# Optimization experiments

Measured on AMD Instinct MI355X. Metric: run time of the kernel, lower is better.

The kernel has to match this reference:

```python
import jax, jax.numpy as jnp
import numpy as np
import math

HIDDEN = 2048
N_HEADS = 16
N_KV_HEADS = 4
HEAD_DIM = HIDDEN // N_HEADS  # 128
MAX_POS = 4096
ROPE_THETA = 10000.0
B, S = 2, 2048


def _rope_tables():
    freqs = 1.0 / (ROPE_THETA ** (np.arange(0, HEAD_DIM, 2, dtype=np.float32) / HEAD_DIM))
    t = np.arange(MAX_POS, dtype=np.float32)
    f = np.outer(t, freqs)                      # [MAX_POS, HEAD_DIM/2]
    emb = np.concatenate([f, f], axis=-1)       # [MAX_POS, HEAD_DIM]
    return jnp.asarray(np.cos(emb)), jnp.asarray(np.sin(emb))


def setup_inputs() -> dict:
    key = jax.random.key(0)
    ks = jax.random.split(key, 8)
    kv_dim = N_KV_HEADS * HEAD_DIM
    cos, sin = _rope_tables()
    return {
        "hidden_states": jax.random.normal(ks[0], (B, S, HIDDEN), jnp.float32),
        "attention_mask": jnp.zeros((B, S), jnp.float32),
        "position_ids": jnp.arange(S, dtype=jnp.int64 if jax.config.read('jax_enable_x64') else jnp.int32)[None, :],
        "q_w": jax.random.normal(ks[1], (HIDDEN, HIDDEN), jnp.float32) * 0.02,
        "q_b": jnp.zeros((HIDDEN,), jnp.float32),
        "k_w": jax.random.normal(ks[2], (kv_dim, HIDDEN), jnp.float32) * 0.02,
        "k_b": jnp.zeros((kv_dim,), jnp.float32),
        "v_w": jax.random.normal(ks[3], (kv_dim, HIDDEN), jnp.float32) * 0.02,
        "v_b": jnp.zeros((kv_dim,), jnp.float32),
        "o_w": jax.random.normal(ks[4], (HIDDEN, HIDDEN), jnp.float32) * 0.02,
        "cos": cos,
        "sin": sin,
    }


def _rotate_half(x):
    x1, x2 = jnp.split(x, 2, axis=-1)
    return jnp.concatenate([-x2, x1], axis=-1)


def reference(hidden_states, attention_mask, position_ids, q_w, q_b, k_w, k_b,
              v_w, v_b, o_w, cos, sin):
    b, s, _ = hidden_states.shape
    # projections (torch Linear: y = x @ W.T + b)
    q = jnp.einsum('bsi,oi->bso', hidden_states, q_w) + q_b
    k = jnp.einsum('bsi,oi->bso', hidden_states, k_w) + k_b
    v = jnp.einsum('bsi,oi->bso', hidden_states, v_w) + v_b
    q = q.reshape(b, s, N_HEADS, HEAD_DIM).transpose(0, 2, 1, 3)      # [b,h,s,d]
    k = k.reshape(b, s, N_KV_HEADS, HEAD_DIM).transpose(0, 2, 1, 3)   # [b,kv,s,d]
    v = v.reshape(b, s, N_KV_HEADS, HEAD_DIM).transpose(0, 2, 1, 3)
    # RoPE: gather per-position cos/sin, broadcast over heads
    c = cos[position_ids][:, None, :, :]   # [1,1,s,d]
    sn = sin[position_ids][:, None, :, :]
    q = q * c + _rotate_half(q) * sn
    k = k * c + _rotate_half(k) * sn
    # GQA: repeat-interleave kv heads to match query heads
    g = N_HEADS // N_KV_HEADS
    k = jnp.repeat(k, g, axis=1)
    v = jnp.repeat(v, g, axis=1)
    scores = jnp.einsum('bhqd,bhkd->bhqk', q, k) / math.sqrt(HEAD_DIM)
    scores = scores + attention_mask[:, None, None, :]
    attn = jax.nn.softmax(scores.astype(jnp.float32), axis=-1).astype(q.dtype)
    out = jnp.einsum('bhqk,bhkd->bhqd', attn, v)
    out = out.transpose(0, 2, 1, 3).reshape(b, s, HIDDEN)
    return jnp.einsum('bsi,oi->bso', out, o_w)
```

## Files before the change

kernel.cpp:

```cpp
#include <hip/hip_runtime.h>

#define HIDDEN 2048
#define NH 16
#define NKV 4
#define HD 128
#define Bb 2
#define Ss 2048
#define TOK 4096
#define KVD 512
#define LOG2E 1.4426950408889634f
#define QSCALE (0.08838834764831845f * 1.4426950408889634f)
#define DEFER 11.54f

typedef short short8 __attribute__((ext_vector_type(8)));
typedef float f32x4 __attribute__((ext_vector_type(4)));
typedef float f32x16 __attribute__((ext_vector_type(16)));
typedef unsigned int uint4v __attribute__((ext_vector_type(4)));

#define AS1 __attribute__((address_space(1)))
#define AS3 __attribute__((address_space(3)))

#define BARRIER() asm volatile("s_barrier" ::: "memory")
#define WAITV8()  asm volatile("s_waitcnt vmcnt(8)" ::: "memory")
#define WAITV0()  asm volatile("s_waitcnt vmcnt(0)" ::: "memory")

__device__ __forceinline__ float exp2fast(float x){ return __builtin_amdgcn_exp2f(x); }

__device__ __forceinline__ float bf2f(unsigned short u){
  union { unsigned int i; float f; } x; x.i = ((unsigned int)u) << 16; return x.f;
}
__device__ __forceinline__ unsigned short f2bf(float f){
  union { float f; unsigned int i; } x; x.f = f;
  unsigned int r = x.i + 0x7FFFu + ((x.i >> 16) & 1u);
  return (unsigned short)(r >> 16);
}
__device__ __forceinline__ unsigned int cvtpk(float a, float b){
  unsigned int r;
  asm("v_cvt_pk_bf16_f32 %0, %1, %2" : "=v"(r) : "v"(a), "v"(b));
  return r;
}
__device__ __forceinline__ void gld_lds16(const void* g, void* l){
  __builtin_amdgcn_global_load_lds((const AS1 void*)g, (AS3 void*)l, 16, 0, 0);
}

#define R0 2097152
#define R1 3145728
#define R2 3407872
#define R3 3670016
#define R4 4718592
__global__ void cvt_all(const float* __restrict__ s0, const float* __restrict__ s1,
                        const float* __restrict__ s2, const float* __restrict__ s3,
                        const float* __restrict__ s4, unsigned short* __restrict__ dst){
  int i = blockIdx.x * 256 + threadIdx.x;
  const float* src; int off;
  if      (i < R0){ src = s0; off = 0;  }
  else if (i < R1){ src = s1; off = R0; }
  else if (i < R2){ src = s2; off = R1; }
  else if (i < R3){ src = s3; off = R2; }
  else            { src = s4; off = R3; }
  float4 v = reinterpret_cast<const float4*>(src)[i - off];
  ushort4 o;
  o.x = f2bf(v.x); o.y = f2bf(v.y); o.z = f2bf(v.z); o.w = f2bf(v.w);
  reinterpret_cast<ushort4*>(dst)[i] = o;
}

__global__ __launch_bounds__(256, 2) void gemm_nt(
    const unsigned short* __restrict__ A,
    const unsigned short* __restrict__ Bw,
    const float* __restrict__ bias,
    const float* __restrict__ bias2,
    unsigned short* __restrict__ Cb,
    float* __restrict__ Cf,
    unsigned short* __restrict__ vT,
    int M, int N, int K, int ldc)
{
  __shared__ unsigned short lds[2][2][128*64];
  const int tid  = threadIdx.x;
  const int lane = tid & 63;
  const int w  = tid >> 6;
  const int wr = w >> 1, wc = w & 1;
  const int row0 = blockIdx.x * 128;
  const int col0 = blockIdx.y * 128;
  const int fr  = lane & 15;
  const int g16 = lane >> 4;
  const int l8  = lane >> 3;
  const int slot = lane & 7;

  const f32x4 vzero = {0.f, 0.f, 0.f, 0.f};
  f32x4 acc[4][4];
#pragma unroll
  for (int m = 0; m < 4; m++)
#pragma unroll
    for (int n = 0; n < 4; n++) acc[m][n] = vzero;

  auto STAGE = [&](int buf, int kt){
#pragma unroll
    for (int i = 0; i < 4; i++){
      int r = w*32 + i*8 + l8;
      gld_lds16(A  + (size_t)(row0 + r)*K + kt*64 + ((slot ^ (r & 7)) << 3),
                &lds[buf][0][w*2048 + i*512 + lane*8]);
    }
#pragma unroll
    for (int i = 0; i < 4; i++){
      int r = w*32 + i*8 + l8;
      gld_lds16(Bw + (size_t)(col0 + r)*K + kt*64 + ((slot ^ (r & 7)) << 3),
                &lds[buf][1][w*2048 + i*512 + lane*8]);
    }
  };

  const int NT = K >> 6;
  STAGE(0, 0);
  STAGE(1, 1);
  WAITV8();
  BARRIER();

  for (int kt = 0; kt < NT; kt++){
    const int cur = kt & 1;
    const unsigned short* Al = &lds[cur][0][0];
    const unsigned short* Bl = &lds[cur][1][0];
#pragma unroll
    for (int ks = 0; ks < 2; ks++){
      short8 af[4], bf[4];
#pragma unroll
      for (int m = 0; m < 4; m++){
        int r = wr*64 + m*16 + fr;
        af[m] = *(const short8*)&Al[r*64 + (((ks*4 + g16) ^ (r & 7)) << 3)];
      }
#pragma unroll
      for (int n = 0; n < 4; n++){
        int r = wc*64 + n*16 + fr;
        bf[n] = *(const short8*)&Bl[r*64 + (((ks*4 + g16) ^ (r & 7)) << 3)];
      }
      __builtin_amdgcn_s_setprio(1);
#pragma unroll
      for (int m = 0; m < 4; m++)
#pragma unroll
        for (int n = 0; n < 4; n++)
          acc[m][n] = __builtin_amdgcn_mfma_f32_16x16x32_bf16(af[m], bf[n], acc[m][n], 0, 0, 0);
      __builtin_amdgcn_s_setprio(0);
    }
    if (kt == NT - 1) break;
    BARRIER();
    if (kt + 2 < NT){
      STAGE(cur, kt + 2);
      WAITV8();
    } else {
      WAITV0();
    }
    BARRIER();
  }

  const int rr = g16 * 4;
#pragma unroll
  for (int n = 0; n < 4; n++){
    int col = col0 + wc*64 + n*16 + fr;
    float bv = 0.f;
    if (bias) bv = (bias2 && col >= 512) ? bias2[col - 512] : bias[col];
    if (vT && col >= 512){
#pragma unroll
      for (int m = 0; m < 4; m++){
        int row = row0 + wr*64 + m*16 + rr;
        ushort4 pk;
        pk.x = f2bf(acc[m][n][0] + bv); pk.y = f2bf(acc[m][n][1] + bv);
        pk.z = f2bf(acc[m][n][2] + bv); pk.w = f2bf(acc[m][n][3] + bv);
        *reinterpret_cast<ushort4*>(&vT[(size_t)(col - 512) * TOK + row]) = pk;
      }
    } else {
#pragma unroll
      for (int m = 0; m < 4; m++){
        int row = row0 + wr*64 + m*16 + rr;
#pragma unroll
        for (int r = 0; r < 4; r++){
          float v = acc[m][n][r] + bv;
          if (Cf) Cf[(size_t)(row + r) * ldc + col] = v;
          else    Cb[(size_t)(row + r) * ldc + col] = f2bf(v);
        }
      }
    }
  }
}

__global__ void rope_kernel(unsigned short* __restrict__ q, unsigned short* __restrict__ k,
                            const int* __restrict__ pos,
                            const float* __restrict__ cosT, const float* __restrict__ sinT)
{
  int idx = blockIdx.x * blockDim.x + threadIdx.x;
  const int qN = TOK * NH * 64;
  if (idx < qN){
    int d  = idx & 63;
    int hh = (idx >> 6) & (NH - 1);
    int t  = idx >> 10;
    int p  = pos[t & (Ss - 1)];
    float c = cosT[p * HD + d], s = sinT[p * HD + d];
    unsigned short* base = q + (size_t)t * HIDDEN + hh * HD;
    float lo = bf2f(base[d]), hi = bf2f(base[d + 64]);
    base[d]      = f2bf((lo * c - hi * s) * QSCALE);
    base[d + 64] = f2bf((hi * c + lo * s) * QSCALE);
  } else {
    int j  = idx - qN;
    int d  = j & 63;
    int hh = (j >> 6) & (NKV - 1);
    int t  = j >> 8;
    int p  = pos[t & (Ss - 1)];
    float c = cosT[p * HD + d], s = sinT[p * HD + d];
    unsigned short* base = k + (size_t)t * KVD + hh * HD;
    float lo = bf2f(base[d]), hi = bf2f(base[d + 64]);
    base[d]      = f2bf(lo * c - hi * s);
    base[d + 64] = f2bf(hi * c + lo * s);
  }
}

__global__ __launch_bounds__(512, 2) void attn_kernel(
    const unsigned short* __restrict__ Q,
    const unsigned short* __restrict__ Kb,
    const unsigned short* __restrict__ Vt,
    const float* __restrict__ mask,
    unsigned short* __restrict__ O)
{
  __shared__ unsigned short Klds[64*128];
  __shared__ unsigned short Vlds[128*64];

  const int tid = threadIdx.x, lane = tid & 63, wid = tid >> 6;
  const int qt = blockIdx.x, kvh = blockIdx.y, b = blockIdx.z;
  const int head = kvh*4 + (wid >> 1);
  const int q0 = lane & 31;
  const int h  = lane >> 5;
  const int tokQ = b*Ss + qt*64 + (wid & 1)*32;

  short8 qf[8];
#pragma unroll
  for (int ds = 0; ds < 8; ds++)
    qf[ds] = *(const short8*)(Q + (size_t)(tokQ + q0)*HIDDEN + head*HD + ds*16 + h*8);

  f32x16 oacc[4];
#pragma unroll
  for (int dblk = 0; dblk < 4; dblk++)
#pragma unroll
    for (int r = 0; r < 16; r++) oacc[dblk][r] = 0.f;
  float mrow = -1e30f, lrow = 0.f;

  const float* maskrow = mask + b*Ss;

  const int kk0 = tid >> 4;
  const int kd  = tid & 15;
  const int dv0 = tid >> 3;
  const int vk  = tid & 7;

  const size_t kgbase = (size_t)(b*Ss)*KVD + (size_t)kvh*HD;
  const size_t vgbase = (size_t)(kvh*HD)*TOK + (size_t)(b*Ss);

  short8 kpre[2], vpre[2];
#pragma unroll
  for (int i = 0; i < 2; i++){
    kpre[i] = *(const short8*)(Kb + kgbase + (size_t)(kk0 + i*32)*KVD + kd*8);
    vpre[i] = *(const short8*)(Vt + vgbase + (size_t)(dv0 + i*64)*TOK + vk*8);
  }

  for (int kt = 0; kt < Ss/64; kt++){
    if (kt) __syncthreads();
#pragma unroll
    for (int i = 0; i < 2; i++){
      int kk = kk0 + i*32;
      *(short8*)&Klds[kk*128 + ((kd*8) ^ ((kk & 7) << 3))] = kpre[i];
      int dv = dv0 + i*64;
      *(short8*)&Vlds[dv*64 + ((vk*8) ^ ((dv & 7) << 3))] = vpre[i];
    }
    __syncthreads();
    if (kt + 1 < Ss/64){
      const int tok = (kt + 1)*64;
#pragma unroll
      for (int i = 0; i < 2; i++){
        kpre[i] = *(const short8*)(Kb + kgbase + (size_t)(tok + kk0 + i*32)*KVD + kd*8);
        vpre[i] = *(const short8*)(Vt + vgbase + (size_t)(dv0 + i*64)*TOK + tok + vk*8);
      }
    }

    f32x16 st0, st1;
#pragma unroll
    for (int r = 0; r < 16; r++){ st0[r] = 0.f; st1[r] = 0.f; }
    __builtin_amdgcn_s_setprio(1);
#pragma unroll
    for (int ds = 0; ds < 8; ds++){
      short8 kf0 = *(const short8*)&Klds[(q0     )*128 + ((ds*16 + h*8) ^ ((q0 & 7) << 3))];
      short8 kf1 = *(const short8*)&Klds[(32 + q0)*128 + ((ds*16 + h*8) ^ ((q0 & 7) << 3))];
      st0 = __builtin_amdgcn_mfma_f32_32x32x16_bf16(kf0, qf[ds], st0, 0, 0, 0);
      st1 = __builtin_amdgcn_mfma_f32_32x32x16_bf16(kf1, qf[ds], st1, 0, 0, 0);
    }
    __builtin_amdgcn_s_setprio(0);

    float p[32];
#pragma unroll
    for (int g2 = 0; g2 < 4; g2++){
      f32x4 m0 = *(const f32x4*)(maskrow + kt*64      + g2*8 + h*4);
      f32x4 m1 = *(const f32x4*)(maskrow + kt*64 + 32 + g2*8 + h*4);
#pragma unroll
      for (int r = 0; r < 4; r++){
        p[g2*4 + r]      = st0[g2*4 + r] + m0[r] * LOG2E;
        p[16 + g2*4 + r] = st1[g2*4 + r] + m1[r] * LOG2E;
      }
    }

    float vmax = p[0];
#pragma unroll
    for (int i = 1; i < 32; i++) vmax = fmaxf(vmax, p[i]);
    vmax = fmaxf(vmax, __shfl_xor(vmax, 32));
    if (__any(vmax > mrow + DEFER)){
      float mnew = fmaxf(mrow, vmax);
      float sc = exp2fast(mrow - mnew);
      mrow = mnew; lrow *= sc;
#pragma unroll
      for (int reg = 0; reg < 16; reg++){
        float scr = __shfl(sc, (reg & 3) + 8*(reg >> 2) + 4*h);
#pragma unroll
        for (int dblk = 0; dblk < 4; dblk++) oacc[dblk][reg] *= scr;
      }
    }
    float rs = 0.f;
#pragma unroll
    for (int i = 0; i < 32; i++){ p[i] = exp2fast(p[i] - mrow); rs += p[i]; }
    rs += __shfl_xor(rs, 32);
    lrow += rs;

    unsigned int pk[8][2];
#pragma unroll
    for (int G = 0; G < 8; G++){
      pk[G][0] = cvtpk(p[G*4 + 0], p[G*4 + 1]);
      pk[G][1] = cvtpk(p[G*4 + 2], p[G*4 + 3]);
    }
    short8 pa[4];
#pragma unroll
    for (int ks = 0; ks < 4; ks++){
      const int ia = 4*(ks >> 1) + 2*(ks & 1);
      unsigned int A0 = pk[ia][0],   A1 = pk[ia][1];
      unsigned int B0 = pk[ia+1][0], B1 = pk[ia+1][1];
      unsigned int s0 = h ? A0 : B0, s1 = h ? A1 : B1;
      unsigned int r0 = (unsigned int)__shfl_xor((int)s0, 32);
      unsigned int r1 = (unsigned int)__shfl_xor((int)s1, 32);
      uint4v w = { h ? r0 : A0, h ? r1 : A1, h ? B0 : r0, h ? B1 : r1 };
      pa[ks] = __builtin_bit_cast(short8, w);
    }

    __builtin_amdgcn_s_setprio(1);
#pragma unroll
    for (int dblk = 0; dblk < 4; dblk++){
#pragma unroll
      for (int ks = 0; ks < 4; ks++){
        short8 vb = *(const short8*)&Vlds[(dblk*32 + q0)*64 + ((ks*16 + h*8) ^ ((q0 & 7) << 3))];
        oacc[dblk] = __builtin_amdgcn_mfma_f32_32x32x16_bf16(pa[ks], vb, oacc[dblk], 0, 0, 0);
      }
    }
    __builtin_amdgcn_s_setprio(0);
  }

  float inv = 1.0f / lrow;
#pragma unroll
  for (int reg = 0; reg < 16; reg++){
    const int crow = (reg & 3) + 8*(reg >> 2) + 4*h;
    float invr = __shfl(inv, crow);
    int row = tokQ + crow;
#pragma unroll
    for (int dblk = 0; dblk < 4; dblk++)
      O[(size_t)row*HIDDEN + head*HD + dblk*32 + q0] = f2bf(oacc[dblk][reg] * invr);
  }
}

extern "C" void kernel_launch(void* const* d_in, const int* in_sizes, int n_in,
                              void* d_out, int out_size, void* d_ws, size_t ws_size,
                              hipStream_t stream)
{
  (void)in_sizes; (void)n_in; (void)out_size; (void)ws_size;
  const float* hs   = (const float*)d_in[0];
  const float* mask = (const float*)d_in[1];
  const int*   pos  = (const int*)d_in[2];
  const float* qw   = (const float*)d_in[3];
  const float* qb   = (const float*)d_in[4];
  const float* kw   = (const float*)d_in[5];
  const float* kb   = (const float*)d_in[6];
  const float* vw   = (const float*)d_in[7];
  const float* vb   = (const float*)d_in[8];
  const float* ow   = (const float*)d_in[9];
  const float* cosT = (const float*)d_in[10];
  const float* sinT = (const float*)d_in[11];
  float* out = (float*)d_out;

  unsigned short* ws  = (unsigned short*)d_ws;
  unsigned short* hsB = ws;
  unsigned short* qwB = hsB + (size_t)TOK * HIDDEN;
  unsigned short* kwB = qwB + (size_t)HIDDEN * HIDDEN;
  unsigned short* vwB = kwB + (size_t)KVD * HIDDEN;
  unsigned short* owB = vwB + (size_t)KVD * HIDDEN;
  unsigned short* qB  = owB + (size_t)HIDDEN * HIDDEN;
  unsigned short* kB  = qB  + (size_t)TOK * HIDDEN;
  unsigned short* vTB = kB  + (size_t)TOK * KVD;
  unsigned short* aoB = vTB + (size_t)KVD * TOK;
  (void)vwB;

  cvt_all<<<R4 / 256, 256, 0, stream>>>(hs, qw, kw, vw, ow, ws);

  gemm_nt<<<dim3(TOK/128, HIDDEN/128), 256, 0, stream>>>(hsB, qwB, qb, nullptr, qB, nullptr, nullptr, TOK, HIDDEN, HIDDEN, HIDDEN);
  gemm_nt<<<dim3(TOK/128, 1024/128),   256, 0, stream>>>(hsB, kwB, kb, vb, kB, nullptr, vTB, TOK, 1024, HIDDEN, KVD);

  {
    int total = TOK * NH * 64 + TOK * NKV * 64;
    rope_kernel<<<total / 256, 256, 0, stream>>>(qB, kB, pos, cosT, sinT);
  }

  attn_kernel<<<dim3(Ss/64, NKV, Bb), 512, 0, stream>>>(qB, kB, vTB, mask, aoB);

  gemm_nt<<<dim3(TOK/128, HIDDEN/128), 256, 0, stream>>>(aoB, owB, nullptr, nullptr, nullptr, out, nullptr, TOK, HIDDEN, HIDDEN, HIDDEN);
}
```

Baseline: 223.8 us.

## Double-buffer K/V tiles in LDS and shrink attention blocks to 32 queries

The attention kernel now uses two LDS buffers for K and V tiles, writing the next tile while computing on the current one. This cuts the per-tile barriers from two to one. Blocks shrink to 4 waves covering 32 query rows across the 4 heads of a KV group, and the grid doubles. This aims to overlap loads with MFMA work, at the cost of twice the LDS per block and twice the K/V global reads per query.

```diff
diff --git a/kernel.cpp b/kernel.cpp
--- a/kernel.cpp
+++ b/kernel.cpp
@@ -210,22 +210,22 @@
   }
 }
 
-__global__ __launch_bounds__(512, 2) void attn_kernel(
+__global__ __launch_bounds__(256, 2) void attn_kernel(
     const unsigned short* __restrict__ Q,
     const unsigned short* __restrict__ Kb,
     const unsigned short* __restrict__ Vt,
     const float* __restrict__ mask,
     unsigned short* __restrict__ O)
 {
-  __shared__ unsigned short Klds[64*128];
-  __shared__ unsigned short Vlds[128*64];
+  __shared__ unsigned short Klds[2][64*128];
+  __shared__ unsigned short Vlds[2][128*64];
 
   const int tid = threadIdx.x, lane = tid & 63, wid = tid >> 6;
   const int qt = blockIdx.x, kvh = blockIdx.y, b = blockIdx.z;
-  const int head = kvh*4 + (wid >> 1);
+  const int head = kvh*4 + wid;
   const int q0 = lane & 31;
   const int h  = lane >> 5;
-  const int tokQ = b*Ss + qt*64 + (wid & 1)*32;
+  const int tokQ = b*Ss + qt*32;
 
   short8 qf[8];
 #pragma unroll
@@ -249,31 +249,34 @@
   const size_t kgbase = (size_t)(b*Ss)*KVD + (size_t)kvh*HD;
   const size_t vgbase = (size_t)(kvh*HD)*TOK + (size_t)(b*Ss);
 
-  short8 kpre[2], vpre[2];
-#pragma unroll
-  for (int i = 0; i < 2; i++){
-    kpre[i] = *(const short8*)(Kb + kgbase + (size_t)(kk0 + i*32)*KVD + kd*8);
-    vpre[i] = *(const short8*)(Vt + vgbase + (size_t)(dv0 + i*64)*TOK + vk*8);
-  }
-
-  for (int kt = 0; kt < Ss/64; kt++){
-    if (kt) __syncthreads();
-#pragma unroll
-    for (int i = 0; i < 2; i++){
-      int kk = kk0 + i*32;
-      *(short8*)&Klds[kk*128 + ((kd*8) ^ ((kk & 7) << 3))] = kpre[i];
-      int dv = dv0 + i*64;
-      *(short8*)&Vlds[dv*64 + ((vk*8) ^ ((dv & 7) << 3))] = vpre[i];
-    }
-    __syncthreads();
-    if (kt + 1 < Ss/64){
-      const int tok = (kt + 1)*64;
-#pragma unroll
-      for (int i = 0; i < 2; i++){
-        kpre[i] = *(const short8*)(Kb + kgbase + (size_t)(tok + kk0 + i*32)*KVD + kd*8);
-        vpre[i] = *(const short8*)(Vt + vgbase + (size_t)(dv0 + i*64)*TOK + tok + vk*8);
-      }
-    }
+  short8 kpre[4], vpre[4];
+  auto LOADREG = [&](int tok){
+#pragma unroll
+    for (int i = 0; i < 4; i++){
+      kpre[i] = *(const short8*)(Kb + kgbase + (size_t)(tok + kk0 + i*16)*KVD + kd*8);
+      vpre[i] = *(const short8*)(Vt + vgbase + (size_t)(dv0 + i*32)*TOK + tok + vk*8);
+    }
+  };
+  auto WRITELDS = [&](int buf){
+#pragma unroll
+    for (int i = 0; i < 4; i++){
+      int kk = kk0 + i*16;
+      *(short8*)&Klds[buf][kk*128 + ((kd*8) ^ ((kk & 7) << 3))] = kpre[i];
+      int dv = dv0 + i*32;
+      *(short8*)&Vlds[buf][dv*64 + ((vk*8) ^ ((dv & 7) << 3))] = vpre[i];
+    }
+  };
+
+  const int NT = Ss/64;
+  LOADREG(0);
+  WRITELDS(0);
+  LOADREG(64);
+  __syncthreads();
+
+  for (int kt = 0; kt < NT; kt++){
+    const int buf = kt & 1;
+    if (kt + 1 < NT) WRITELDS(buf ^ 1);
+    if (kt + 2 < NT) LOADREG((kt + 2)*64);
 
     f32x16 st0, st1;
 #pragma unroll
@@ -281,8 +284,8 @@
     __builtin_amdgcn_s_setprio(1);
 #pragma unroll
     for (int ds = 0; ds < 8; ds++){
-      short8 kf0 = *(const short8*)&Klds[(q0     )*128 + ((ds*16 + h*8) ^ ((q0 & 7) << 3))];
-      short8 kf1 = *(const short8*)&Klds[(32 + q0)*128 + ((ds*16 + h*8) ^ ((q0 & 7) << 3))];
+      short8 kf0 = *(const short8*)&Klds[buf][(q0     )*128 + ((ds*16 + h*8) ^ ((q0 & 7) << 3))];
+      short8 kf1 = *(const short8*)&Klds[buf][(32 + q0)*128 + ((ds*16 + h*8) ^ ((q0 & 7) << 3))];
       st0 = __builtin_amdgcn_mfma_f32_32x32x16_bf16(kf0, qf[ds], st0, 0, 0, 0);
       st1 = __builtin_amdgcn_mfma_f32_32x32x16_bf16(kf1, qf[ds], st1, 0, 0, 0);
     }
@@ -345,11 +348,13 @@
     for (int dblk = 0; dblk < 4; dblk++){
 #pragma unroll
       for (int ks = 0; ks < 4; ks++){
-        short8 vb = *(const short8*)&Vlds[(dblk*32 + q0)*64 + ((ks*16 + h*8) ^ ((q0 & 7) << 3))];
+        short8 vb = *(const short8*)&Vlds[buf][(dblk*32 + q0)*64 + ((ks*16 + h*8) ^ ((q0 & 7) << 3))];
         oacc[dblk] = __builtin_amdgcn_mfma_f32_32x32x16_bf16(pa[ks], vb, oacc[dblk], 0, 0, 0);
       }
     }
     __builtin_amdgcn_s_setprio(0);
+
+    __syncthreads();
   }
 
   float inv = 1.0f / lrow;
@@ -405,7 +410,7 @@
     rope_kernel<<<total / 256, 256, 0, stream>>>(qB, kB, pos, cosT, sinT);
   }
 
-  attn_kernel<<<dim3(Ss/64, NKV, Bb), 512, 0, stream>>>(qB, kB, vTB, mask, aoB);
+  attn_kernel<<<dim3(Ss/32, NKV, Bb), 256, 0, stream>>>(qB, kB, vTB, mask, aoB);
 
   gemm_nt<<<dim3(TOK/128, HIDDEN/128), 256, 0, stream>>>(aoB, owB, nullptr, nullptr, nullptr, out, nullptr, TOK, HIDDEN, HIDDEN, HIDDEN);
 }
```

New measurement: 224.3 us. Within noise of the previous version (+0.3%).
